# Optimization experiments

Measured on AMD Instinct MI355X. Metric: run time of the kernel, lower is better.

Reference implementation:

```python
import jax, jax.numpy as jnp
import numpy as np

SKIP = 2
EPS = 1e-9
K_PEN = 0.01
MU_BG = 0.0
VAR_BG = 100.0
SIZ = (256, 256, 256)
SIZA = (160, 192, 160)
NC = 10
COMPS = np.array([2, 2, 1, 1, 2, 1, 1, 2, 1])
NG = int(COMPS.sum())  # 13
FSIZ = (13, 13, 13)  # round(256*1.0/20)


def setup_inputs() -> dict:
    key = jax.random.key(0)
    ks = jax.random.split(key, 10)
    I = jax.random.uniform(ks[0], SIZ, jnp.float32)
    A = jax.random.uniform(ks[1], (*SIZA, NC), jnp.float32)
    A = A / jnp.sum(A, axis=-1, keepdims=True)  # probabilistic atlas
    aff_I = jnp.eye(4, dtype=jnp.float32)
    aff_A = jnp.diag(jnp.array([SIZ[0] / SIZA[0], SIZ[1] / SIZA[1], SIZ[2] / SIZA[2], 1.0], jnp.float32))
    mus = jax.random.uniform(ks[2], (NG,), jnp.float32)
    vars_ = 0.05 + 0.1 * jax.random.uniform(ks[3], (NG,), jnp.float32)
    w = np.asarray(jax.random.uniform(ks[4], (NG,))) + 0.1
    cls = np.repeat(np.arange(len(COMPS)), COMPS)
    onehot = (cls[:, None] == np.arange(len(COMPS))[None, :]).astype(np.float32)
    w = w / (onehot @ (onehot.T @ w))  # weights sum to 1 within each class
    weights = jnp.asarray(w, jnp.float32)
    gmm_onehot = jnp.asarray(onehot)
    ts = 0.5 * jax.random.normal(ks[5], (3,), jnp.float32)
    thetas = 2.0 * jax.random.normal(ks[6], (3,), jnp.float32)  # degrees
    scalings = 0.5 * jax.random.normal(ks[7], (3,), jnp.float32)
    shears = 0.5 * jax.random.normal(ks[8], (3,), jnp.float32)
    FIELD = 0.5 * jax.random.normal(ks[9], (*FSIZ, 3), jnp.float32)
    return dict(I=I, A=A, aff_I=aff_I, aff_A=aff_A, mus=mus, vars_=vars_, weights=weights,
                gmm_onehot=gmm_onehot, ts=ts, thetas=thetas, scalings=scalings,
                shears=shears, FIELD=FIELD)


def _bspline3(t):
    t = jnp.abs(t)
    return jnp.where(t < 1, (4.0 - 6.0 * t * t + 3.0 * t * t * t) / 6.0,
                     jnp.where(t < 2, (2.0 - t) ** 3 / 6.0, 0.0))


def _cubic_matrix(coords, n):
    # dense [m, n] cubic-B-spline sampling matrix with circular (dft) boundary,
    # prefilter=False (FIELD values treated as spline coefficients)
    m = coords.shape[0]
    base = jnp.floor(coords).astype(jnp.int32)
    W = jnp.zeros((m, n), coords.dtype)
    rows = jnp.arange(m)
    for k in (-1, 0, 1, 2):
        node = base + k
        W = W.at[rows, node % n].add(_bspline3(coords - node))
    return W


def reference(I, A, aff_I, aff_A, mus, vars_, weights, gmm_onehot, ts, thetas, scalings, shears, FIELD):
    nxA, nyA, nzA, C = A.shape
    fx, fy, fz = FIELD.shape[:3]
    dt = I.dtype

    # ---- affine from parameters (T @ Sh @ Sc @ Rz @ Ry @ Rx) ----
    th = thetas * (jnp.pi / 180.0)
    sh = shears / 100.0
    sc = jnp.exp(scalings / 20.0)
    c, s = jnp.cos(th), jnp.sin(th)
    Rx = jnp.array([[1.0, 0.0, 0.0, 0.0], [0.0, c[0], -s[0], 0.0], [0.0, s[0], c[0], 0.0], [0.0, 0.0, 0.0, 1.0]])
    Ry = jnp.array([[c[1], 0.0, s[1], 0.0], [0.0, 1.0, 0.0, 0.0], [-s[1], 0.0, c[1], 0.0], [0.0, 0.0, 0.0, 1.0]])
    Rz = jnp.array([[c[2], -s[2], 0.0, 0.0], [s[2], c[2], 0.0, 0.0], [0.0, 0.0, 1.0, 0.0], [0.0, 0.0, 0.0, 1.0]])
    Sc = jnp.diag(jnp.concatenate([sc, jnp.ones((1,), sc.dtype)]))
    Sh = jnp.array([[1.0, sh[1], sh[2], 0.0], [sh[0], 1.0, sh[2], 0.0], [sh[0], sh[1], 1.0, 0.0], [0.0, 0.0, 0.0, 1.0]])
    T = jnp.eye(4, dtype=dt).at[:3, 3].set(ts)
    AFF = T @ Sh @ Sc @ Rz @ Ry @ Rx
    V = jnp.linalg.inv(AFF @ aff_A) @ aff_I  # image voxel -> atlas voxel

    # ---- cubic-spline resample of deformation field (separable grid) ----
    xs = jnp.arange(0, I.shape[0], SKIP).astype(dt)
    ys = jnp.arange(0, I.shape[1], SKIP).astype(dt)
    zs = jnp.arange(0, I.shape[2], SKIP).astype(dt)
    field_f = FIELD / 100.0 * jnp.array([nxA, nyA, nzA], dt)  # [fx,fy,fz,3]
    Wx = _cubic_matrix(fx * xs / I.shape[0], fx)
    Wy = _cubic_matrix(fy * ys / I.shape[1], fy)
    Wz = _cubic_matrix(fz * zs / I.shape[2], fz)
    t1 = jnp.einsum('ia,abcd->ibcd', Wx, field_f)
    t1 = jnp.einsum('jb,ibcd->ijcd', Wy, t1)
    field_rs = jnp.einsum('kc,ijcd->ijkd', Wz, t1)  # [X,Y,Z,3]

    X = xs[:, None, None]
    Y = ys[None, :, None]
    Z = zs[None, None, :]
    gx = V[0, 0] * X + V[0, 1] * Y + V[0, 2] * Z + V[0, 3] + field_rs[..., 0]
    gy = V[1, 0] * X + V[1, 1] * Y + V[1, 2] * Z + V[1, 3] + field_rs[..., 1]
    gz = V[2, 0] * X + V[2, 1] * Y + V[2, 2] * Z + V[2, 3] + field_rs[..., 2]

    # ---- trilinear pull of atlas (zero bound, no extrapolation) ----
    x0 = jnp.floor(gx).astype(jnp.int32); rx = gx - x0
    y0 = jnp.floor(gy).astype(jnp.int32); ry = gy - y0
    z0 = jnp.floor(gz).astype(jnp.int32); rz = gz - z0
    Af = A.reshape(-1, C)
    acc = jnp.zeros((*gx.shape, C), dt)
    for dx in (0, 1):
        ix = x0 + dx; wx = rx if dx else 1.0 - rx
        vx = (ix >= 0) & (ix < nxA); ixc = jnp.clip(ix, 0, nxA - 1)
        for dy in (0, 1):
            iy = y0 + dy; wy = ry if dy else 1.0 - ry
            vy = (iy >= 0) & (iy < nyA); iyc = jnp.clip(iy, 0, nyA - 1)
            for dz in (0, 1):
                iz = z0 + dz; wz = rz if dz else 1.0 - rz
                vz = (iz >= 0) & (iz < nzA); izc = jnp.clip(iz, 0, nzA - 1)
                w = jnp.where(vx & vy & vz, wx * wy * wz, 0.0)
                flat = (ixc * nyA + iyc) * nzA + izc
                vals = jnp.take(Af, flat.reshape(-1), axis=0).reshape(*flat.shape, C)
                acc = acc + w[..., None] * vals

    atlas_rs = jnp.clip(acc, 0.0, 1.0)
    missing = 1.0 - jnp.sum(atlas_rs, axis=-1)
    prior_bg = jnp.clip(atlas_rs[..., 0] + missing, 0.0, 1.0)
    priors_rest = atlas_rs[..., 1:]  # already clipped to [0,1]
    priors = jnp.concatenate([prior_bg[..., None], priors_rest], axis=-1)

    # ---- GMM likelihoods ----
    Iskip = I[::SKIP, ::SKIP, ::SKIP]
    gl_bg = jnp.exp(-0.5 * (Iskip - MU_BG) ** 2 / VAR_BG) / jnp.sqrt(2.0 * jnp.pi * VAR_BG)
    gl = jnp.exp(-0.5 * (Iskip[..., None] - mus) ** 2 / vars_) / jnp.sqrt(2.0 * jnp.pi * vars_)  # [X,Y,Z,NG]
    class_lh = jnp.einsum('xyzg,gc->xyzc', weights * gl, gmm_onehot)  # per-class mixture
    normalizer = prior_bg * gl_bg + jnp.sum(priors_rest * class_lh, axis=-1)
    log_lh = jnp.log(EPS + normalizer)

    # ---- gradient penalty on field in voxel units of the full image grid ----
    siz_vec = jnp.array(I.shape, dt)
    fsiz_vec = jnp.array(FIELD.shape[:3], dt)
    fv = field_f * (fsiz_vec / siz_vec)
    pen = (jnp.mean((fv[1:] - fv[:-1]) ** 2)
           + jnp.mean((fv[:, 1:] - fv[:, :-1]) ** 2)
           + jnp.mean((fv[:, :, 1:] - fv[:, :, :-1]) ** 2)) / 3.0
    def_pen = K_PEN * pen
    loss = -jnp.mean(log_lh) + def_pen
    grids_new = jnp.stack([gx, gy, gz], axis=-1)
    return (loss, grids_new, priors, def_pen)
```

## Files before the change

kernel.cpp:

```cpp
#include <hip/hip_runtime.h>

#define PI_D 3.14159265358979323846
#define NS 128
#define NVOX (NS*NS*NS)
#define NBLK (NVOX/256)


static __device__ __forceinline__ float bspline3f(float t) {
    t = fabsf(t);
    if (t < 1.0f) return (4.0f - 6.0f*t*t + 3.0f*t*t*t) * (1.0f/6.0f);
    if (t < 2.0f) { float u = 2.0f - t; return u*u*u * (1.0f/6.0f); }
    return 0.0f;
}

static __device__ void mm4(const double* Am, const double* Bm, double* Cm) {
    for (int i = 0; i < 4; i++)
        for (int j = 0; j < 4; j++) {
            double s = 0.0;
            for (int k = 0; k < 4; k++) s += Am[i*4+k] * Bm[k*4+j];
            Cm[i*4+j] = s;
        }
}

static __device__ void inv4(const double* Am, double* Om) {
    double a[4][8];
    for (int i = 0; i < 4; i++)
        for (int j = 0; j < 4; j++) {
            a[i][j]   = Am[i*4+j];
            a[i][4+j] = (i == j) ? 1.0 : 0.0;
        }
    for (int col = 0; col < 4; col++) {
        int piv = col; double best = fabs(a[col][col]);
        for (int r = col+1; r < 4; r++) {
            double v = fabs(a[r][col]);
            if (v > best) { best = v; piv = r; }
        }
        if (piv != col)
            for (int j = 0; j < 8; j++) { double t = a[col][j]; a[col][j] = a[piv][j]; a[piv][j] = t; }
        double d = a[col][col];
        for (int j = 0; j < 8; j++) a[col][j] /= d;
        for (int r = 0; r < 4; r++) if (r != col) {
            double f = a[r][col];
            for (int j = 0; j < 8; j++) a[r][j] -= f * a[col][j];
        }
    }
    for (int i = 0; i < 4; i++)
        for (int j = 0; j < 4; j++) Om[i*4+j] = a[i][4+j];
}


__global__ void AD_prep(const float* __restrict__ aff_I, const float* __restrict__ aff_A,
                        const float* __restrict__ ts, const float* __restrict__ thetas,
                        const float* __restrict__ scalings, const float* __restrict__ shears,
                        const float* __restrict__ FIELD,
                        const float* __restrict__ vars_, const float* __restrict__ weights,
                        const float* __restrict__ mus,
                        float* __restrict__ wsf, int* __restrict__ wsi)
{
    const int tid = threadIdx.x;

    if (tid == 0) {
        double c0 = cos((double)thetas[0]*(PI_D/180.0)), s0 = sin((double)thetas[0]*(PI_D/180.0));
        double c1 = cos((double)thetas[1]*(PI_D/180.0)), s1 = sin((double)thetas[1]*(PI_D/180.0));
        double c2 = cos((double)thetas[2]*(PI_D/180.0)), s2 = sin((double)thetas[2]*(PI_D/180.0));
        double Rx[16] = {1,0,0,0,  0,c0,-s0,0,  0,s0,c0,0,  0,0,0,1};
        double Ry[16] = {c1,0,s1,0,  0,1,0,0,  -s1,0,c1,0,  0,0,0,1};
        double Rz[16] = {c2,-s2,0,0,  s2,c2,0,0,  0,0,1,0,  0,0,0,1};
        double t1[16], t2[16];
        mm4(Ry, Rx, t1);
        mm4(Rz, t1, t2);
        double sc0 = exp((double)scalings[0]/20.0);
        double sc1 = exp((double)scalings[1]/20.0);
        double sc2 = exp((double)scalings[2]/20.0);
        for (int j = 0; j < 4; j++) { t2[0*4+j] *= sc0; t2[1*4+j] *= sc1; t2[2*4+j] *= sc2; }
        double sh0 = (double)shears[0]/100.0, sh1 = (double)shears[1]/100.0, sh2 = (double)shears[2]/100.0;
        double Sh[16] = {1,sh1,sh2,0,  sh0,1,sh2,0,  sh0,sh1,1,0,  0,0,0,1};
        mm4(Sh, t2, t1);
        t1[3]  += (double)ts[0];
        t1[7]  += (double)ts[1];
        t1[11] += (double)ts[2];
        double Aa[16]; for (int i = 0; i < 16; i++) Aa[i] = (double)aff_A[i];
        mm4(t1, Aa, t2);
        double Mi[16]; inv4(t2, Mi);
        double Ai[16]; for (int i = 0; i < 16; i++) Ai[i] = (double)aff_I[i];
        mm4(Mi, Ai, t1);
        for (int i = 0; i < 16; i++) wsf[i] = (float)t1[i];
    }

    if (tid < 13) {
        float va = vars_[tid];
        wsf[17+tid] = weights[tid] / sqrtf(6.283185307179586f * va);
        wsf[32+tid] = -0.5f / va;
        wsf[48+tid] = mus[tid];
    }

    if (tid < 128) {
        for (int a = 0; a < 3; a++) {
            float coord = (13.0f * (float)(2*tid)) / 256.0f;
            int base = (int)floorf(coord);
            for (int k = 0; k < 4; k++) {
                int node = base + (k - 1);
                float w = bspline3f(coord - (float)node);
                int idx = node % 13; if (idx < 0) idx += 13;
                wsf[64 + (a*128+tid)*4 + k] = w;
                wsi[(a*128+tid)*4 + k] = idx;
            }
        }
    }

    __shared__ double red[256];
    double s = 0.0;
    for (int i = tid; i < 12*13*13*3; i += 256) {
        int d = i % 3; int r = i / 3; int cc = r % 13; r /= 13; int b = r % 13; int a = r / 13;
        float sf = (d == 1) ? 0.0975f : 0.08125f;
        float f1 = FIELD[(((a+1)*13+b)*13+cc)*3+d] * sf;
        float f0 = FIELD[(((a  )*13+b)*13+cc)*3+d] * sf;
        float df = f1 - f0; s += (double)(df*df);
    }
    for (int i = tid; i < 13*12*13*3; i += 256) {
        int d = i % 3; int r = i / 3; int cc = r % 13; r /= 13; int b = r % 12; int a = r / 12;
        float sf = (d == 1) ? 0.0975f : 0.08125f;
        float f1 = FIELD[((a*13+(b+1))*13+cc)*3+d] * sf;
        float f0 = FIELD[((a*13+(b  ))*13+cc)*3+d] * sf;
        float df = f1 - f0; s += (double)(df*df);
    }
    for (int i = tid; i < 13*13*12*3; i += 256) {
        int d = i % 3; int r = i / 3; int cc = r % 12; r /= 12; int b = r % 13; int a = r / 13;
        float sf = (d == 1) ? 0.0975f : 0.08125f;
        float f1 = FIELD[((a*13+b)*13+(cc+1))*3+d] * sf;
        float f0 = FIELD[((a*13+b)*13+(cc  ))*3+d] * sf;
        float df = f1 - f0; s += (double)(df*df);
    }
    red[tid] = s; __syncthreads();
    for (int st = 128; st > 0; st >>= 1) {
        if (tid < st) red[tid] += red[tid+st];
        __syncthreads();
    }
    if (tid == 0) wsf[16] = (float)(0.01 * red[0] / (6084.0 * 3.0));
}

__global__ void AD_field(const float* __restrict__ FIELD,
                         const float* __restrict__ wsf, const int* __restrict__ wsi,
                         float* __restrict__ tB)
{
    __shared__ float fld[13*13*13*3];
    const int tid = threadIdx.x;
    for (int i = tid; i < 13*13*13*3; i += 256) {
        int d = i - (i/3)*3;
        float sc = (d == 1) ? 1.92f : 1.6f;
        fld[i] = FIELD[i] * sc;
    }
    __syncthreads();

    const int p = blockIdx.x*256 + tid;
    const int j = p & 127, i = p >> 7;

    const float4 wx = *(const float4*)(wsf + 64 + (0*128+i)*4);
    const float4 wy = *(const float4*)(wsf + 64 + (1*128+j)*4);
    const int4  ix4 = *(const int4*)(wsi + (0*128+i)*4);
    const int4  iy4 = *(const int4*)(wsi + (1*128+j)*4);
    const float wxa[4] = {wx.x, wx.y, wx.z, wx.w};
    const float wya[4] = {wy.x, wy.y, wy.z, wy.w};
    const int   ixa[4] = {ix4.x, ix4.y, ix4.z, ix4.w};
    const int   iya[4] = {iy4.x, iy4.y, iy4.z, iy4.w};

    float acc[39];
    #pragma unroll
    for (int t = 0; t < 39; t++) acc[t] = 0.f;

    #pragma unroll
    for (int a = 0; a < 4; a++) {
        #pragma unroll
        for (int b = 0; b < 4; b++) {
            const float wab = wxa[a] * wya[b];
            const float* src = fld + (ixa[a]*13 + iya[b]) * 39;
            #pragma unroll
            for (int t = 0; t < 39; t++) acc[t] = fmaf(wab, src[t], acc[t]);
        }
    }
    float* dst = tB + (size_t)p * 39;
    #pragma unroll
    for (int t = 0; t < 39; t++) dst[t] = acc[t];
}

__launch_bounds__(256)
__global__ void AD_main(const float* __restrict__ I, const float* __restrict__ A,
                        const float* __restrict__ wsf, const int* __restrict__ wsi,
                        const float* __restrict__ tB,
                        double* __restrict__ partials, float* __restrict__ out)
{
    __shared__ float sh[80];
    __shared__ double wred[4];
    const int tid = threadIdx.x;

    {
        const float* src = tB + (size_t)(blockIdx.x * 2) * 39;
        if (tid < 78) sh[tid] = src[tid];
    }
    __syncthreads();

    const int v = blockIdx.x*256 + tid;
    const int z = v & 127, y = (v >> 7) & 127, x = v >> 14;

    const float4 wzv = *(const float4*)(wsf + 64 + (2*128+z)*4);
    const int4  izv = *(const int4*)(wsi + (2*128+z)*4);
    const float* myrow = sh + (tid >> 7) * 39;

    float fr0, fr1, fr2;
    {
        const float* r0 = myrow + izv.x*3;
        const float* r1 = myrow + izv.y*3;
        const float* r2 = myrow + izv.z*3;
        const float* r3 = myrow + izv.w*3;
        fr0 = wzv.x*r0[0] + wzv.y*r1[0] + wzv.z*r2[0] + wzv.w*r3[0];
        fr1 = wzv.x*r0[1] + wzv.y*r1[1] + wzv.z*r2[1] + wzv.w*r3[1];
        fr2 = wzv.x*r0[2] + wzv.y*r1[2] + wzv.z*r2[2] + wzv.w*r3[2];
    }

    const float X = (float)(2*x), Yf = (float)(2*y), Zf = (float)(2*z);
    const float gx = wsf[0]*X + wsf[1]*Yf + wsf[2]*Zf  + wsf[3]  + fr0;
    const float gy = wsf[4]*X + wsf[5]*Yf + wsf[6]*Zf  + wsf[7]  + fr1;
    const float gz = wsf[8]*X + wsf[9]*Yf + wsf[10]*Zf + wsf[11] + fr2;

    float* grids = out + 1;
    __builtin_nontemporal_store(gx, grids + (size_t)v*3 + 0);
    __builtin_nontemporal_store(gy, grids + (size_t)v*3 + 1);
    __builtin_nontemporal_store(gz, grids + (size_t)v*3 + 2);

    float acc[10];
    #pragma unroll
    for (int c = 0; c < 10; c++) acc[c] = 0.f;

    const float x0f = floorf(gx), y0f = floorf(gy), z0f = floorf(gz);
    const int x0 = (int)x0f, y0 = (int)y0f, z0 = (int)z0f;
    const float rx = gx - x0f, ry = gy - y0f, rz = gz - z0f;

    #pragma unroll
    for (int dx = 0; dx < 2; dx++) {
        const int ixq = x0 + dx; const float wxq = dx ? rx : 1.f - rx;
        const bool vxq = (ixq >= 0) && (ixq < 160);
        const int ixc = ixq < 0 ? 0 : (ixq > 159 ? 159 : ixq);
        #pragma unroll
        for (int dy = 0; dy < 2; dy++) {
            const int iyq = y0 + dy; const float wyq = dy ? ry : 1.f - ry;
            const bool vyq = (iyq >= 0) && (iyq < 192);
            const int iyc = iyq < 0 ? 0 : (iyq > 191 ? 191 : iyq);
            #pragma unroll
            for (int dz = 0; dz < 2; dz++) {
                const int izq = z0 + dz; const float wzq = dz ? rz : 1.f - rz;
                const bool vzq = (izq >= 0) && (izq < 160);
                const int izc = izq < 0 ? 0 : (izq > 159 ? 159 : izq);
                const float w = (vxq && vyq && vzq) ? wxq*wyq*wzq : 0.f;
                const float2* ap = (const float2*)(A + ((size_t)(ixc*192 + iyc)*160 + izc)*10);
                #pragma unroll
                for (int h = 0; h < 5; h++) {
                    float2 t = ap[h];
                    acc[2*h]   = fmaf(w, t.x, acc[2*h]);
                    acc[2*h+1] = fmaf(w, t.y, acc[2*h+1]);
                }
            }
        }
    }

    float pri[10]; float sum = 0.f;
    #pragma unroll
    for (int c = 0; c < 10; c++) {
        float t = acc[c]; t = t < 0.f ? 0.f : (t > 1.f ? 1.f : t);
        pri[c] = t; sum += t;
    }
    float p0 = pri[0] + (1.0f - sum);
    pri[0] = p0 < 0.f ? 0.f : (p0 > 1.f ? 1.f : p0);

    float* priors = out + 1 + (size_t)NVOX*3 + (size_t)v*10;
    #pragma unroll
    for (int c = 0; c < 10; c++) __builtin_nontemporal_store(pri[c], priors + c);

    const float Iv = __builtin_nontemporal_load(I + ((size_t)(2*x)*256 + (size_t)(2*y))*256 + (size_t)(2*z));
    const float gl_bg = expf(-0.005f*Iv*Iv) * 0.039894228040143274f;

    constexpr int CLS[13] = {0,0,1,1,2,3,4,4,5,6,7,7,8};
    float lh[9];
    #pragma unroll
    for (int c = 0; c < 9; c++) lh[c] = 0.f;
    #pragma unroll
    for (int g = 0; g < 13; g++) {
        const float dlt = Iv - wsf[48+g];
        lh[CLS[g]] += wsf[17+g] * expf(dlt*dlt*wsf[32+g]);
    }
    float nrm = pri[0] * gl_bg;
    #pragma unroll
    for (int c = 0; c < 9; c++) nrm = fmaf(pri[c+1], lh[c], nrm);
    const float ll = logf(1e-9f + nrm);

    double s = (double)ll;
    #pragma unroll
    for (int off = 32; off > 0; off >>= 1) s += __shfl_down(s, off, 64);
    if ((tid & 63) == 0) wred[tid >> 6] = s;
    __syncthreads();
    if (tid == 0) partials[blockIdx.x] = (wred[0] + wred[1]) + (wred[2] + wred[3]);
}

__global__ void AD_fin(const double* __restrict__ partials, const float* __restrict__ wsf,
                       float* __restrict__ out, int out_size)
{
    __shared__ double red[256];
    const int tid = threadIdx.x;
    double s = 0.0;
    for (int i = tid; i < NBLK; i += 256) s += partials[i];
    red[tid] = s; __syncthreads();
    for (int st = 128; st > 0; st >>= 1) {
        if (tid < st) red[tid] += red[tid+st];
        __syncthreads();
    }
    if (tid == 0) {
        float dp = wsf[16];
        out[0] = (float)(-(red[0] / (double)NVOX) + (double)dp);
        out[out_size-1] = dp;
    }
}

extern "C" void kernel_launch(void* const* d_in, const int* in_sizes, int n_in,
                              void* d_out, int out_size, void* d_ws, size_t ws_size,
                              hipStream_t stream)
{
    const float* I        = (const float*)d_in[0];
    const float* A        = (const float*)d_in[1];
    const float* aff_I    = (const float*)d_in[2];
    const float* aff_A    = (const float*)d_in[3];
    const float* mus      = (const float*)d_in[4];
    const float* vars_    = (const float*)d_in[5];
    const float* weights  = (const float*)d_in[6];
    const float* ts       = (const float*)d_in[8];
    const float* thetas   = (const float*)d_in[9];
    const float* scalings = (const float*)d_in[10];
    const float* shears   = (const float*)d_in[11];
    const float* FIELD    = (const float*)d_in[12];

    float* out = (float*)d_out;
    float* wsf = (float*)d_ws;
    int*   wsi = (int*)(wsf + 1600);
    double* partials = (double*)((char*)d_ws + 16384);
    float* tB = (float*)((char*)d_ws + 131072);

    hipLaunchKernelGGL(AD_prep, dim3(1), dim3(256), 0, stream,
                       aff_I, aff_A, ts, thetas, scalings, shears, FIELD, vars_, weights, mus, wsf, wsi);
    hipLaunchKernelGGL(AD_field, dim3(64), dim3(256), 0, stream,
                       FIELD, wsf, wsi, tB);
    hipLaunchKernelGGL(AD_main, dim3(NBLK), dim3(256), 0, stream,
                       I, A, wsf, wsi, tB, partials, out);
    hipLaunchKernelGGL(AD_fin, dim3(1), dim3(256), 0, stream,
                       partials, wsf, out, out_size);
}
```

Before: 130.9 us.

## Tile voxels into 3D blocks and stage atlas neighborhood in shared memory

Each block now covers an 8x4x8 voxel tile instead of a linear z-row segment. The block finds its bounding box of atlas indices with a wavefront shuffle plus shared atomics, loads that box cooperatively into LDS, and does the trilinear gather from LDS. It falls back to global gathers when the box exceeds the fixed size. The aim is to turn scattered uncoalesced 8-corner global loads into coalesced loads with reuse, at the cost of extra syncs, more LDS (which may limit occupancy), and reordered output writes.

```diff
diff --git a/kernel.cpp b/kernel.cpp
--- a/kernel.cpp
+++ b/kernel.cpp
@@ -4,6 +4,10 @@
 #define NS 128
 #define NVOX (NS*NS*NS)
 #define NBLK (NVOX/256)
+
+#define BX 13
+#define BY 8
+#define BZ 13
 
 
 static __device__ __forceinline__ float bspline3f(float t) {
@@ -189,22 +193,45 @@
                         const float* __restrict__ tB,
                         double* __restrict__ partials, float* __restrict__ out)
 {
-    __shared__ float sh[80];
+    __shared__ float box[BX*BY*BZ*10];
+    __shared__ float tbrow[32*40];
     __shared__ double wred[4];
+    __shared__ int mm[6];
+
     const int tid = threadIdx.x;
+    const int bid = blockIdx.x;
+    const int tz = bid & 15, ty = (bid >> 4) & 31, tx = bid >> 9;
 
     {
-        const float* src = tB + (size_t)(blockIdx.x * 2) * 39;
-        if (tid < 78) sh[tid] = src[tid];
+        float tr[5];
+        #pragma unroll
+        for (int k = 0; k < 5; k++) {
+            int i = k*256 + tid;
+            if (i < 32*39) {
+                int r = i / 39, o = i - r*39;
+                tr[k] = tB[(size_t)((tx*8 + (r>>2))*128 + ty*4 + (r&3))*39 + o];
+            }
+        }
+        if (tid < 3) mm[tid] = 0x7fffffff;
+        else if (tid < 6) mm[tid] = 0;
+        #pragma unroll
+        for (int k = 0; k < 5; k++) {
+            int i = k*256 + tid;
+            if (i < 32*39) {
+                int r = i / 39, o = i - r*39;
+                tbrow[r*40 + o] = tr[k];
+            }
+        }
     }
     __syncthreads();
 
-    const int v = blockIdx.x*256 + tid;
-    const int z = v & 127, y = (v >> 7) & 127, x = v >> 14;
+    const int dz = tid & 7, dy = (tid >> 3) & 3, dxv = tid >> 5;
+    const int x = tx*8 + dxv, y = ty*4 + dy, z = tz*8 + dz;
+    const int v = (x << 14) + (y << 7) + z;
 
     const float4 wzv = *(const float4*)(wsf + 64 + (2*128+z)*4);
     const int4  izv = *(const int4*)(wsi + (2*128+z)*4);
-    const float* myrow = sh + (tid >> 7) * 39;
+    const float* myrow = tbrow + (dxv*4 + dy)*40;
 
     float fr0, fr1, fr2;
     {
@@ -227,36 +254,111 @@
     __builtin_nontemporal_store(gy, grids + (size_t)v*3 + 1);
     __builtin_nontemporal_store(gz, grids + (size_t)v*3 + 2);
 
-    float acc[10];
-    #pragma unroll
-    for (int c = 0; c < 10; c++) acc[c] = 0.f;
-
     const float x0f = floorf(gx), y0f = floorf(gy), z0f = floorf(gz);
     const int x0 = (int)x0f, y0 = (int)y0f, z0 = (int)z0f;
     const float rx = gx - x0f, ry = gy - y0f, rz = gz - z0f;
 
-    #pragma unroll
-    for (int dx = 0; dx < 2; dx++) {
-        const int ixq = x0 + dx; const float wxq = dx ? rx : 1.f - rx;
-        const bool vxq = (ixq >= 0) && (ixq < 160);
-        const int ixc = ixq < 0 ? 0 : (ixq > 159 ? 159 : ixq);
-        #pragma unroll
-        for (int dy = 0; dy < 2; dy++) {
-            const int iyq = y0 + dy; const float wyq = dy ? ry : 1.f - ry;
-            const bool vyq = (iyq >= 0) && (iyq < 192);
-            const int iyc = iyq < 0 ? 0 : (iyq > 191 ? 191 : iyq);
+    int lx[2], ly[2], lz[2]; float wxt[2], wyt[2], wzt[2];
+    lx[0] = x0   < 0 ? 0 : (x0   > 159 ? 159 : x0);
+    lx[1] = x0+1 < 0 ? 0 : (x0+1 > 159 ? 159 : x0+1);
+    ly[0] = y0   < 0 ? 0 : (y0   > 191 ? 191 : y0);
+    ly[1] = y0+1 < 0 ? 0 : (y0+1 > 191 ? 191 : y0+1);
+    lz[0] = z0   < 0 ? 0 : (z0   > 159 ? 159 : z0);
+    lz[1] = z0+1 < 0 ? 0 : (z0+1 > 159 ? 159 : z0+1);
+    wxt[0] = (x0   >= 0 && x0   < 160) ? (1.f - rx) : 0.f;
+    wxt[1] = (x0+1 >= 0 && x0+1 < 160) ? rx : 0.f;
+    wyt[0] = (y0   >= 0 && y0   < 192) ? (1.f - ry) : 0.f;
+    wyt[1] = (y0+1 >= 0 && y0+1 < 192) ? ry : 0.f;
+    wzt[0] = (z0   >= 0 && z0   < 160) ? (1.f - rz) : 0.f;
+    wzt[1] = (z0+1 >= 0 && z0+1 < 160) ? rz : 0.f;
+
+    {
+        int a0 = lx[0], a1 = ly[0], a2 = lz[0], a3 = lx[1], a4 = ly[1], a5 = lz[1];
+        #pragma unroll
+        for (int off = 32; off > 0; off >>= 1) {
+            a0 = min(a0, __shfl_xor(a0, off, 64));
+            a1 = min(a1, __shfl_xor(a1, off, 64));
+            a2 = min(a2, __shfl_xor(a2, off, 64));
+            a3 = max(a3, __shfl_xor(a3, off, 64));
+            a4 = max(a4, __shfl_xor(a4, off, 64));
+            a5 = max(a5, __shfl_xor(a5, off, 64));
+        }
+        if ((tid & 63) == 0) {
+            atomicMin(&mm[0], a0); atomicMin(&mm[1], a1); atomicMin(&mm[2], a2);
+            atomicMax(&mm[3], a3); atomicMax(&mm[4], a4); atomicMax(&mm[5], a5);
+        }
+    }
+    __syncthreads();
+
+    const int x0b = mm[0], y0b = mm[1], z0b = mm[2];
+    const int sx = mm[3] - x0b + 1, sy = mm[4] - y0b + 1, sz = mm[5] - z0b + 1;
+
+    float acc[10];
+    #pragma unroll
+    for (int c = 0; c < 10; c++) acc[c] = 0.f;
+
+    const float2* A2 = (const float2*)A;
+
+    if (sx <= BX && sy <= BY && sz <= BZ) {
+        const int rn2 = sz * 5;
+        const int n2  = sx * sy * rn2;
+        float2* lds2 = (float2*)box;
+        for (int ibase = 0; ibase < n2; ibase += 256*8) {
+            float2 r[8];
             #pragma unroll
-            for (int dz = 0; dz < 2; dz++) {
-                const int izq = z0 + dz; const float wzq = dz ? rz : 1.f - rz;
-                const bool vzq = (izq >= 0) && (izq < 160);
-                const int izc = izq < 0 ? 0 : (izq > 159 ? 159 : izq);
-                const float w = (vxq && vyq && vzq) ? wxq*wyq*wzq : 0.f;
-                const float2* ap = (const float2*)(A + ((size_t)(ixc*192 + iyc)*160 + izc)*10);
+            for (int k = 0; k < 8; k++) {
+                int i = ibase + k*256 + tid;
+                if (i < n2) {
+                    int row = i / rn2, o = i - row*rn2;
+                    int bx = row / sy, by = row - bx*sy;
+                    r[k] = A2[(size_t)(((x0b+bx)*192 + (y0b+by))*160 + z0b)*5 + o];
+                }
+            }
+            #pragma unroll
+            for (int k = 0; k < 8; k++) {
+                int i = ibase + k*256 + tid;
+                if (i < n2) lds2[i] = r[k];
+            }
+        }
+        __syncthreads();
+
+        const float2* lds2c = (const float2*)box;
+        #pragma unroll
+        for (int ta = 0; ta < 2; ta++) {
+            #pragma unroll
+            for (int tb = 0; tb < 2; tb++) {
+                const float wab = wxt[ta] * wyt[tb];
+                const int rowb = ((lx[ta]-x0b)*sy + (ly[tb]-y0b))*sz - z0b;
                 #pragma unroll
-                for (int h = 0; h < 5; h++) {
-                    float2 t = ap[h];
-                    acc[2*h]   = fmaf(w, t.x, acc[2*h]);
-                    acc[2*h+1] = fmaf(w, t.y, acc[2*h+1]);
+                for (int tc = 0; tc < 2; tc++) {
+                    const float w = wab * wzt[tc];
+                    const float2* p = lds2c + (size_t)(rowb + lz[tc])*5;
+                    #pragma unroll
+                    for (int h = 0; h < 5; h++) {
+                        float2 t = p[h];
+                        acc[2*h]   = fmaf(w, t.x, acc[2*h]);
+                        acc[2*h+1] = fmaf(w, t.y, acc[2*h+1]);
+                    }
+                }
+            }
+        }
+    } else {
+        #pragma unroll
+        for (int ta = 0; ta < 2; ta++) {
+            #pragma unroll
+            for (int tb = 0; tb < 2; tb++) {
+                const float wab = wxt[ta] * wyt[tb];
+                const size_t rowb = (size_t)(lx[ta]*192 + ly[tb]) * 160;
+                #pragma unroll
+                for (int tc = 0; tc < 2; tc++) {
+                    const float w = wab * wzt[tc];
+                    const float2* p = A2 + (rowb + lz[tc])*5;
+                    #pragma unroll
+                    for (int h = 0; h < 5; h++) {
+                        float2 t = p[h];
+                        acc[2*h]   = fmaf(w, t.x, acc[2*h]);
+                        acc[2*h+1] = fmaf(w, t.y, acc[2*h+1]);
+                    }
                 }
             }
         }
```

New measurement: 256.6 us. 96.1% more time.
